# Kernel optimization log

Measured on AMD Instinct MI355X. Metric: run time of the kernel, lower is better.

Reference implementation:

```python
import jax, jax.numpy as jnp
import numpy as np

N_NODES = 50000
N_EDGES = 800000
IN_DIM = 128
HID = 64
HEADS = 4
OUT_DIM = 20
NUM_GRAPHS = 64
NEG_SLOPE = 0.2  # PyG GATConv default leaky_relu slope


def _xavier(key, shape):
    fan_in, fan_out = shape[-1], shape[0]
    lim = float(np.sqrt(6.0 / (fan_in + fan_out)))
    return jax.random.uniform(key, shape, jnp.float32, -lim, lim)


def setup_inputs() -> dict:
    key = jax.random.key(0)
    ks = jax.random.split(key, 12)
    x = jax.random.normal(ks[0], (N_NODES, IN_DIM), jnp.float32)
    edge_index = jax.random.randint(ks[1], (2, N_EDGES), 0, N_NODES, jnp.int32)
    batch = jnp.sort(jax.random.randint(ks[2], (N_NODES,), 0, NUM_GRAPHS, jnp.int32))
    return {
        "x": x,
        "edge_index": edge_index,
        "batch": batch,
        # conv1: in -> HEADS*HID, concat
        "W1": _xavier(ks[3], (HEADS * HID, IN_DIM)),
        "a_src1": _xavier(ks[4], (HEADS, HID)),
        "a_dst1": _xavier(ks[5], (HEADS, HID)),
        "b1": jnp.zeros((HEADS * HID,), jnp.float32),
        # conv2: HEADS*HID -> HID, 1 head
        "W2": _xavier(ks[6], (HID, HEADS * HID)),
        "a_src2": _xavier(ks[7], (1, HID)),
        "a_dst2": _xavier(ks[8], (1, HID)),
        "b2": jnp.zeros((HID,), jnp.float32),
        "fc_W": _xavier(ks[9], (OUT_DIM, HID)),
        "fc_b": jnp.zeros((OUT_DIM,), jnp.float32),
    }


def _gat_conv(x, src, dst, W, a_src, a_dst, b, heads):
    """PyG GATConv: linear -> per-edge LeakyReLU attention -> softmax over
    incoming edges of each target node -> weighted scatter-sum. Self-loops
    are already included in (src, dst). Dropout omitted (eval mode)."""
    n = x.shape[0]
    h = (x @ W.T).reshape(n, heads, -1)            # [N, H, C]
    alpha_s = jnp.einsum("nhc,hc->nh", h, a_src)   # [N, H]
    alpha_d = jnp.einsum("nhc,hc->nh", h, a_dst)
    e = jax.nn.leaky_relu(alpha_s[src] + alpha_d[dst], NEG_SLOPE)  # [E, H]
    # numerically stable segment softmax over dst
    e_max = jax.ops.segment_max(e, dst, num_segments=n)
    e = jnp.exp(e - e_max[dst])
    denom = jax.ops.segment_sum(e, dst, num_segments=n)
    alpha = e / (denom[dst] + 1e-16)               # [E, H]
    msg = h[src] * alpha[..., None]                # [E, H, C]
    out = jax.ops.segment_sum(msg, dst, num_segments=n)  # [N, H, C]
    return out.reshape(n, -1) + b                  # concat heads


def reference(x, edge_index, batch, W1, a_src1, a_dst1, b1,
              W2, a_src2, a_dst2, b2, fc_W, fc_b):
    n = x.shape[0]
    loops = jnp.arange(n, dtype=edge_index.dtype)
    src = jnp.concatenate([edge_index[0], loops])  # add self-loops (PyG default)
    dst = jnp.concatenate([edge_index[1], loops])
    h = jax.nn.elu(_gat_conv(x, src, dst, W1, a_src1, a_dst1, b1, HEADS))
    h = jax.nn.elu(_gat_conv(h, src, dst, W2, a_src2, a_dst2, b2, 1))
    pooled = jax.ops.segment_max(h, batch, num_segments=NUM_GRAPHS)  # [G, HID]
    return pooled @ fc_W.T + fc_b                  # [G, OUT_DIM]
```

## Files before the change

### kernel.cpp

```cpp
#include <hip/hip_runtime.h>
#include <hip/hip_bf16.h>

#define N_NODES_C 50000
#define N_EDGES_C 800000
#define IN_DIM_C  128
#define HID_C     64
#define HEADS_C   4
#define OUT_DIM_C 20
#define NUM_GRAPHS_C 64
#define NEG_SLOPE 0.2f
#define SCAN_BLOCKS 196

typedef __attribute__((ext_vector_type(8))) short bf16x8;
typedef __attribute__((ext_vector_type(4))) float f32x4;
typedef __attribute__((ext_vector_type(2))) float f32x2;

__device__ __forceinline__ float lrelu(float t){ return t > 0.f ? t : NEG_SLOPE*t; }
__device__ __forceinline__ float elu1(float t){ return t > 0.f ? t : __expf(t)-1.f; }
__device__ __forceinline__ ushort f2bf(float f){
  unsigned u = __float_as_uint(f);
  return (ushort)((u + 0x7fffu + ((u>>16)&1u)) >> 16);
}
__device__ __forceinline__ float bflo(unsigned u){ return __uint_as_float(u<<16); }
__device__ __forceinline__ float bfhi(unsigned u){ return __uint_as_float(u & 0xffff0000u); }
__device__ __forceinline__ float bfs(ushort u){ return __uint_as_float(((unsigned)u)<<16); }

__global__ void hist_kernel(const int* __restrict__ ei, int* __restrict__ cursor){
  int e = blockIdx.x*256 + threadIdx.x;
  if (e < N_EDGES_C) atomicAdd(&cursor[ei[N_EDGES_C + e]], 1);
}

__global__ __launch_bounds__(256) void reduce_counts(const int* __restrict__ cursor, int* __restrict__ blockSums){
  int i = blockIdx.x*256 + threadIdx.x;
  int c = (i < N_NODES_C) ? cursor[i] : 0;
  #pragma unroll
  for(int d=32; d>=1; d>>=1) c += __shfl_xor(c, d);
  __shared__ int s4[4];
  int lane = threadIdx.x & 63, wv = threadIdx.x >> 6;
  if(lane==0) s4[wv] = c;
  __syncthreads();
  if(threadIdx.x==0) blockSums[blockIdx.x] = s4[0]+s4[1]+s4[2]+s4[3];
}

__global__ __launch_bounds__(256) void scan_sums(int* __restrict__ blockSums){
  __shared__ int sh[256];
  int t = threadIdx.x;
  int v = (t < SCAN_BLOCKS) ? blockSums[t] : 0;
  sh[t] = v; __syncthreads();
  #pragma unroll
  for(int off=1; off<256; off<<=1){
    int u = (t>=off) ? sh[t-off] : 0;
    __syncthreads();
    sh[t] += u;
    __syncthreads();
  }
  if(t < SCAN_BLOCKS) blockSums[t] = sh[t] - v;
}

__global__ __launch_bounds__(256) void scan_block(int* __restrict__ cursor, const int* __restrict__ blockSums,
                                                  int* __restrict__ offsets){
  __shared__ int sh[256];
  int t = threadIdx.x;
  int i = blockIdx.x*256 + t;
  int c = (i < N_NODES_C) ? cursor[i] : 0;
  sh[t] = c; __syncthreads();
  #pragma unroll
  for(int off=1; off<256; off<<=1){
    int u = (t>=off) ? sh[t-off] : 0;
    __syncthreads();
    sh[t] += u;
    __syncthreads();
  }
  int excl = sh[t] - c;
  int pref = blockSums[blockIdx.x] + excl;
  if(i < N_NODES_C){
    offsets[i] = pref;
    cursor[i]  = pref;
    if(i == N_NODES_C-1) offsets[N_NODES_C] = pref + c;
  }
}

__global__ void fill_kernel(const int* __restrict__ ei, int* __restrict__ cursor,
                            int* __restrict__ adj){
  int e = blockIdx.x*256 + threadIdx.x;
  if (e >= N_EDGES_C) return;
  int sI = ei[e]; int d = ei[N_EDGES_C + e];
  int p = atomicAdd(&cursor[d], 1);
  adj[p] = sI;
}

__global__ __launch_bounds__(256) void wperm_kernel(const float* __restrict__ W1, const float* __restrict__ W2,
    ushort* __restrict__ Wp1h, ushort* __restrict__ Wp1l,
    ushort* __restrict__ Wp2h, ushort* __restrict__ Wp2l){
  int i = blockIdx.x*256 + threadIdx.x;
  const float* src; ushort *dh, *dl; int gidx;
  if(i < 4096){
    int kc = i>>10, oc = (i>>6)&15, l = i&63;
    src = W1 + (size_t)(oc*16 + (l&15))*IN_DIM_C + kc*32 + (l>>4)*8;
    dh = Wp1h; dl = Wp1l; gidx = i;
  } else if(i < 4096+2048){
    int i2 = i - 4096;
    int kc = i2>>8, oc = (i2>>6)&3, l = i2&63;
    src = W2 + (size_t)(oc*16 + (l&15))*256 + kc*32 + (l>>4)*8;
    dh = Wp2h; dl = Wp2l; gidx = i2;
  } else return;
  ushort h8[8], l8[8];
  #pragma unroll
  for(int j=0;j<8;j++){
    float f = src[j];
    ushort h = f2bf(f);
    h8[j] = h; l8[j] = f2bf(f - bfs(h));
  }
  #pragma unroll
  for(int j=0;j<8;j++){ dh[gidx*8+j] = h8[j]; dl[gidx*8+j] = l8[j]; }
}

#define HS1_STRIDE 260
__global__ __launch_bounds__(256) void lin1_mfma(const float* __restrict__ x,
    const ushort* __restrict__ Wp1h, const ushort* __restrict__ Wp1l,
    const float* __restrict__ aS, const float* __restrict__ aD,
    ushort* __restrict__ h1, float* __restrict__ as1, float* __restrict__ ad1){
  __shared__ ushort hs[64*HS1_STRIDE];
  int t = threadIdx.x, w = t>>6, l = t&63;
  int n0b = blockIdx.x*64;
  int n0 = n0b + w*16;
  bool active = (n0 < N_NODES_C);
  int row = l & 15, kg = l >> 4;
  if(active){
    bf16x8 ah[4], al[4];
    int gn = n0 + row; if(gn > N_NODES_C-1) gn = N_NODES_C-1;
    const float* xrow = x + (size_t)gn*IN_DIM_C + kg*8;
    #pragma unroll
    for(int kc=0;kc<4;kc++){
      float4 f0 = *(const float4*)(xrow + kc*32);
      float4 f1 = *(const float4*)(xrow + kc*32 + 4);
      float fv[8] = {f0.x,f0.y,f0.z,f0.w,f1.x,f1.y,f1.z,f1.w};
      #pragma unroll
      for(int j=0;j<8;j++){
        ushort h = f2bf(fv[j]);
        float r = fv[j] - bfs(h);
        ah[kc][j] = (short)h;
        al[kc][j] = (short)f2bf(r);
      }
    }
    const bf16x8* Wh = (const bf16x8*)Wp1h + l;
    const bf16x8* Wl = (const bf16x8*)Wp1l + l;
    f32x4 acc[16];
    #pragma unroll
    for(int oc=0;oc<16;oc++){
      f32x4 a = {0.f,0.f,0.f,0.f};
      const bf16x8* ph = Wh + oc*64;
      const bf16x8* pl = Wl + oc*64;
      #pragma unroll
      for(int kc=0;kc<4;kc++){
        bf16x8 bh = ph[kc*1024];
        bf16x8 bl = pl[kc*1024];
        a = __builtin_amdgcn_mfma_f32_16x16x32_bf16(ah[kc], bh, a, 0, 0, 0);
        a = __builtin_amdgcn_mfma_f32_16x16x32_bf16(ah[kc], bl, a, 0, 0, 0);
        a = __builtin_amdgcn_mfma_f32_16x16x32_bf16(al[kc], bh, a, 0, 0, 0);
      }
      acc[oc] = a;
    }
    #pragma unroll
    for(int h=0;h<4;h++){
      float ps0=0.f,ps1=0.f,ps2=0.f,ps3=0.f, pd0=0.f,pd1=0.f,pd2=0.f,pd3=0.f;
      #pragma unroll
      for(int oi=0;oi<4;oi++){
        int oc = h*4 + oi;
        float as_ = aS[oc*16 + row];
        float ad_ = aD[oc*16 + row];
        ps0 = fmaf(acc[oc][0], as_, ps0); pd0 = fmaf(acc[oc][0], ad_, pd0);
        ps1 = fmaf(acc[oc][1], as_, ps1); pd1 = fmaf(acc[oc][1], ad_, pd1);
        ps2 = fmaf(acc[oc][2], as_, ps2); pd2 = fmaf(acc[oc][2], ad_, pd2);
        ps3 = fmaf(acc[oc][3], as_, ps3); pd3 = fmaf(acc[oc][3], ad_, pd3);
      }
      #pragma unroll
      for(int d=1; d<16; d<<=1){
        ps0 += __shfl_xor(ps0,d); ps1 += __shfl_xor(ps1,d);
        ps2 += __shfl_xor(ps2,d); ps3 += __shfl_xor(ps3,d);
        pd0 += __shfl_xor(pd0,d); pd1 += __shfl_xor(pd1,d);
        pd2 += __shfl_xor(pd2,d); pd3 += __shfl_xor(pd3,d);
      }
      if(row==0){
        int nb4 = (n0 + kg*4)*4 + h;
        as1[nb4+0] = ps0; as1[nb4+4] = ps1; as1[nb4+8] = ps2; as1[nb4+12] = ps3;
        ad1[nb4+0] = pd0; ad1[nb4+4] = pd1; ad1[nb4+8] = pd2; ad1[nb4+12] = pd3;
      }
    }
    #pragma unroll
    for(int oc=0;oc<16;oc++){
      #pragma unroll
      for(int r=0;r<4;r++){
        hs[(w*16 + kg*4 + r)*HS1_STRIDE + oc*16 + row] = f2bf(acc[oc][r]);
      }
    }
  }
  __syncthreads();
  int nvalid = N_NODES_C - n0b; if(nvalid > 64) nvalid = 64;
  for(int i=t; i<nvalid*32; i+=256){
    int r = i>>5, c = i&31;
    ((uint4*)(h1 + (size_t)(n0b+r)*256))[c] = *(const uint4*)(hs + r*HS1_STRIDE + c*8);
  }
}

__global__ __launch_bounds__(256) void agg1_kernel(const int* __restrict__ offsets, const int* __restrict__ adj,
    const ushort* __restrict__ h1,
    const float* __restrict__ as1, const float* __restrict__ ad1,
    const float* __restrict__ b1, float* __restrict__ out1){
  int wv = threadIdx.x>>6, lane = threadIdx.x&63;
  int v = blockIdx.x*4 + wv;
  int head = lane>>4;
  int start = offsets[v], end = offsets[v+1];
  float adh = ad1[(v<<2)+head];
  float ash = as1[(v<<2)+head];
  float wself = __expf(lrelu(ash+adh));
  float denom = wself;
  const char* hb = (const char*)h1;
  unsigned loff = ((unsigned)lane)<<3;
  uint2 pv = *(const uint2*)(hb + ((((unsigned)v)<<9) + loff));
  f32x2 acc01 = {wself*bflo(pv.x), wself*bfhi(pv.x)};
  f32x2 acc23 = {wself*bflo(pv.y), wself*bfhi(pv.y)};
  int i = start;
  for(; i+8 <= end; i += 8){
    int s0 = adj[i],   s1 = adj[i+1], s2 = adj[i+2], s3 = adj[i+3];
    int s4 = adj[i+4], s5 = adj[i+5], s6 = adj[i+6], s7 = adj[i+7];
    float a0 = as1[(s0<<2)+head], a1 = as1[(s1<<2)+head];
    float a2 = as1[(s2<<2)+head], a3 = as1[(s3<<2)+head];
    float a4 = as1[(s4<<2)+head], a5 = as1[(s5<<2)+head];
    float a6 = as1[(s6<<2)+head], a7 = as1[(s7<<2)+head];
    uint2 p0 = *(const uint2*)(hb + ((((unsigned)s0)<<9) + loff));
    uint2 p1 = *(const uint2*)(hb + ((((unsigned)s1)<<9) + loff));
    uint2 p2 = *(const uint2*)(hb + ((((unsigned)s2)<<9) + loff));
    uint2 p3 = *(const uint2*)(hb + ((((unsigned)s3)<<9) + loff));
    uint2 p4 = *(const uint2*)(hb + ((((unsigned)s4)<<9) + loff));
    uint2 p5 = *(const uint2*)(hb + ((((unsigned)s5)<<9) + loff));
    uint2 p6 = *(const uint2*)(hb + ((((unsigned)s6)<<9) + loff));
    uint2 p7 = *(const uint2*)(hb + ((((unsigned)s7)<<9) + loff));
    float w0 = __expf(lrelu(a0+adh)), w1 = __expf(lrelu(a1+adh));
    float w2 = __expf(lrelu(a2+adh)), w3 = __expf(lrelu(a3+adh));
    float w4 = __expf(lrelu(a4+adh)), w5 = __expf(lrelu(a5+adh));
    float w6 = __expf(lrelu(a6+adh)), w7 = __expf(lrelu(a7+adh));
    denom += ((w0+w1)+(w2+w3)) + ((w4+w5)+(w6+w7));
    f32x2 W;
    W.x = w0; W.y = w0;
    acc01 = __builtin_elementwise_fma(W, (f32x2){bflo(p0.x), bfhi(p0.x)}, acc01);
    acc23 = __builtin_elementwise_fma(W, (f32x2){bflo(p0.y), bfhi(p0.y)}, acc23);
    W.x = w1; W.y = w1;
    acc01 = __builtin_elementwise_fma(W, (f32x2){bflo(p1.x), bfhi(p1.x)}, acc01);
    acc23 = __builtin_elementwise_fma(W, (f32x2){bflo(p1.y), bfhi(p1.y)}, acc23);
    W.x = w2; W.y = w2;
    acc01 = __builtin_elementwise_fma(W, (f32x2){bflo(p2.x), bfhi(p2.x)}, acc01);
    acc23 = __builtin_elementwise_fma(W, (f32x2){bflo(p2.y), bfhi(p2.y)}, acc23);
    W.x = w3; W.y = w3;
    acc01 = __builtin_elementwise_fma(W, (f32x2){bflo(p3.x), bfhi(p3.x)}, acc01);
    acc23 = __builtin_elementwise_fma(W, (f32x2){bflo(p3.y), bfhi(p3.y)}, acc23);
    W.x = w4; W.y = w4;
    acc01 = __builtin_elementwise_fma(W, (f32x2){bflo(p4.x), bfhi(p4.x)}, acc01);
    acc23 = __builtin_elementwise_fma(W, (f32x2){bflo(p4.y), bfhi(p4.y)}, acc23);
    W.x = w5; W.y = w5;
    acc01 = __builtin_elementwise_fma(W, (f32x2){bflo(p5.x), bfhi(p5.x)}, acc01);
    acc23 = __builtin_elementwise_fma(W, (f32x2){bflo(p5.y), bfhi(p5.y)}, acc23);
    W.x = w6; W.y = w6;
    acc01 = __builtin_elementwise_fma(W, (f32x2){bflo(p6.x), bfhi(p6.x)}, acc01);
    acc23 = __builtin_elementwise_fma(W, (f32x2){bflo(p6.y), bfhi(p6.y)}, acc23);
    W.x = w7; W.y = w7;
    acc01 = __builtin_elementwise_fma(W, (f32x2){bflo(p7.x), bfhi(p7.x)}, acc01);
    acc23 = __builtin_elementwise_fma(W, (f32x2){bflo(p7.y), bfhi(p7.y)}, acc23);
  }
  for(; i < end; i++){
    int s0 = adj[i];
    float a0 = as1[(s0<<2)+head];
    uint2 p0 = *(const uint2*)(hb + ((((unsigned)s0)<<9) + loff));
    float w0 = __expf(lrelu(a0+adh));
    denom += w0;
    f32x2 W; W.x = w0; W.y = w0;
    acc01 = __builtin_elementwise_fma(W, (f32x2){bflo(p0.x), bfhi(p0.x)}, acc01);
    acc23 = __builtin_elementwise_fma(W, (f32x2){bflo(p0.y), bfhi(p0.y)}, acc23);
  }
  float inv = 1.f/(denom + 1e-16f);
  float4 bv = *(const float4*)(b1 + (lane<<2));
  float4 r;
  r.x = elu1(acc01.x*inv + bv.x);
  r.y = elu1(acc01.y*inv + bv.y);
  r.z = elu1(acc23.x*inv + bv.z);
  r.w = elu1(acc23.y*inv + bv.w);
  *(float4*)(out1 + ((size_t)v<<8) + (lane<<2)) = r;
}

#define HS2_STRIDE 68
__global__ __launch_bounds__(256) void lin2_mfma(const float* __restrict__ in,
    const ushort* __restrict__ Wp2h, const ushort* __restrict__ Wp2l,
    const float* __restrict__ aS, const float* __restrict__ aD,
    ushort* __restrict__ h2, float* __restrict__ as2, float* __restrict__ ad2){
  __shared__ ushort hs[64*HS2_STRIDE];
  int t = threadIdx.x, w = t>>6, l = t&63;
  int n0b = blockIdx.x*64;
  int n0 = n0b + w*16;
  bool active = (n0 < N_NODES_C);
  int row = l & 15, kg = l >> 4;
  if(active){
    bf16x8 ah[8], al[8];
    int gn = n0 + row; if(gn > N_NODES_C-1) gn = N_NODES_C-1;
    const float* xrow = in + (size_t)gn*256 + kg*8;
    #pragma unroll
    for(int kc=0;kc<8;kc++){
      float4 f0 = *(const float4*)(xrow + kc*32);
      float4 f1 = *(const float4*)(xrow + kc*32 + 4);
      float fv[8] = {f0.x,f0.y,f0.z,f0.w,f1.x,f1.y,f1.z,f1.w};
      #pragma unroll
      for(int j=0;j<8;j++){
        ushort h = f2bf(fv[j]);
        float r = fv[j] - bfs(h);
        ah[kc][j] = (short)h;
        al[kc][j] = (short)f2bf(r);
      }
    }
    const bf16x8* Wh = (const bf16x8*)Wp2h + l;
    const bf16x8* Wl = (const bf16x8*)Wp2l + l;
    f32x4 acc[4];
    #pragma unroll
    for(int oc=0;oc<4;oc++){
      f32x4 a = {0.f,0.f,0.f,0.f};
      const bf16x8* ph = Wh + oc*64;
      const bf16x8* pl = Wl + oc*64;
      #pragma unroll
      for(int kc=0;kc<8;kc++){
        bf16x8 bh = ph[kc*256];
        bf16x8 bl = pl[kc*256];
        a = __builtin_amdgcn_mfma_f32_16x16x32_bf16(ah[kc], bh, a, 0, 0, 0);
        a = __builtin_amdgcn_mfma_f32_16x16x32_bf16(ah[kc], bl, a, 0, 0, 0);
        a = __builtin_amdgcn_mfma_f32_16x16x32_bf16(al[kc], bh, a, 0, 0, 0);
      }
      acc[oc] = a;
    }
    {
      float ps0=0.f,ps1=0.f,ps2=0.f,ps3=0.f, pd0=0.f,pd1=0.f,pd2=0.f,pd3=0.f;
      #pragma unroll
      for(int oc=0;oc<4;oc++){
        float as_ = aS[oc*16 + row];
        float ad_ = aD[oc*16 + row];
        ps0 = fmaf(acc[oc][0], as_, ps0); pd0 = fmaf(acc[oc][0], ad_, pd0);
        ps1 = fmaf(acc[oc][1], as_, ps1); pd1 = fmaf(acc[oc][1], ad_, pd1);
        ps2 = fmaf(acc[oc][2], as_, ps2); pd2 = fmaf(acc[oc][2], ad_, pd2);
        ps3 = fmaf(acc[oc][3], as_, ps3); pd3 = fmaf(acc[oc][3], ad_, pd3);
      }
      #pragma unroll
      for(int d=1; d<16; d<<=1){
        ps0 += __shfl_xor(ps0,d); ps1 += __shfl_xor(ps1,d);
        ps2 += __shfl_xor(ps2,d); ps3 += __shfl_xor(ps3,d);
        pd0 += __shfl_xor(pd0,d); pd1 += __shfl_xor(pd1,d);
        pd2 += __shfl_xor(pd2,d); pd3 += __shfl_xor(pd3,d);
      }
      if(row==0){
        int n = n0 + kg*4;
        as2[n+0] = ps0; as2[n+1] = ps1; as2[n+2] = ps2; as2[n+3] = ps3;
        ad2[n+0] = pd0; ad2[n+1] = pd1; ad2[n+2] = pd2; ad2[n+3] = pd3;
      }
    }
    #pragma unroll
    for(int oc=0;oc<4;oc++){
      #pragma unroll
      for(int r=0;r<4;r++){
        hs[(w*16 + kg*4 + r)*HS2_STRIDE + oc*16 + row] = f2bf(acc[oc][r]);
      }
    }
  }
  __syncthreads();
  int nvalid = N_NODES_C - n0b; if(nvalid > 64) nvalid = 64;
  for(int i=t; i<nvalid*8; i+=256){
    int r = i>>3, c = i&7;
    ((uint4*)(h2 + (size_t)(n0b+r)*64))[c] = *(const uint4*)(hs + r*HS2_STRIDE + c*8);
  }
}

__global__ __launch_bounds__(256) void agg2_kernel(const int* __restrict__ offsets, const int* __restrict__ adj,
    const ushort* __restrict__ h2,
    const float* __restrict__ as2, const float* __restrict__ ad2,
    const float* __restrict__ b2, float* __restrict__ out2){
  int wv = threadIdx.x>>6, lane = threadIdx.x&63;
  int v = blockIdx.x*4 + wv;
  int half = lane>>5, sl = lane&31;
  int start = offsets[v], end = offsets[v+1];
  float adv = ad2[v], asv = as2[v];
  float wself = __expf(lrelu(asv+adv));
  const unsigned* hu = (const unsigned*)h2;
  float denom = half ? 0.f : wself;
  f32x2 acc = {0.f, 0.f};
  if(!half){
    unsigned us = hu[(((unsigned)v)<<5) + sl];
    acc.x = wself*bflo(us); acc.y = wself*bfhi(us);
  }
  int i = start + half;
  for(; i+2 < end; i += 4){
    int sA = adj[i], sB = adj[i+2];
    float aA = as2[sA], aB = as2[sB];
    unsigned uA = hu[(((unsigned)sA)<<5) + sl];
    unsigned uB = hu[(((unsigned)sB)<<5) + sl];
    float wA = __expf(lrelu(aA+adv));
    float wB = __expf(lrelu(aB+adv));
    denom += wA + wB;
    f32x2 W;
    W.x = wA; W.y = wA;
    acc = __builtin_elementwise_fma(W, (f32x2){bflo(uA), bfhi(uA)}, acc);
    W.x = wB; W.y = wB;
    acc = __builtin_elementwise_fma(W, (f32x2){bflo(uB), bfhi(uB)}, acc);
  }
  for(; i < end; i += 2){
    int s = adj[i];
    float wg = __expf(lrelu(as2[s]+adv));
    unsigned u = hu[(((unsigned)s)<<5) + sl];
    denom += wg;
    f32x2 W; W.x = wg; W.y = wg;
    acc = __builtin_elementwise_fma(W, (f32x2){bflo(u), bfhi(u)}, acc);
  }
  acc.x += __shfl_xor(acc.x, 32);
  acc.y += __shfl_xor(acc.y, 32);
  denom += __shfl_xor(denom, 32);
  if(!half){
    float inv = 1.f/(denom + 1e-16f);
    float2 bv = *(const float2*)(b2 + sl*2);
    float2 r;
    r.x = elu1(acc.x*inv + bv.x);
    r.y = elu1(acc.y*inv + bv.y);
    *(float2*)(out2 + (((size_t)v)<<6) + sl*2) = r;
  }
}

__global__ __launch_bounds__(256) void pool_fc_kernel(const float* __restrict__ out2, const int* __restrict__ batch,
    const float* __restrict__ fcW, const float* __restrict__ fcb, float* __restrict__ out){
  int g = blockIdx.x;
  int tid=threadIdx.x; int c = tid&63; int slot = tid>>6;
  int lo=0, hi=N_NODES_C;
  while(lo<hi){ int mid=(lo+hi)>>1; if(batch[mid] < g) lo=mid+1; else hi=mid; }
  int start=lo;
  hi=N_NODES_C;
  while(lo<hi){ int mid=(lo+hi)>>1; if(batch[mid] < g+1) lo=mid+1; else hi=mid; }
  int end=lo;
  float mm = -INFINITY;
  #pragma unroll 4
  for(int n=start+slot; n<end; n+=4) mm = fmaxf(mm, out2[(size_t)n*64+c]);
  __shared__ float sred[4][64];
  sred[slot][c]=mm;
  __syncthreads();
  if(tid < 64){
    float p = fmaxf(fmaxf(sred[0][tid],sred[1][tid]), fmaxf(sred[2][tid],sred[3][tid]));
    sred[0][tid]=p;
  }
  __syncthreads();
  if(tid < OUT_DIM_C){
    float acc = fcb[tid];
    #pragma unroll
    for(int cc=0;cc<64;cc++) acc = fmaf(sred[0][cc], fcW[tid*64+cc], acc);
    out[g*OUT_DIM_C + tid] = acc;
  }
}

extern "C" void kernel_launch(void* const* d_in, const int* in_sizes, int n_in,
                              void* d_out, int out_size, void* d_ws, size_t ws_size,
                              hipStream_t stream) {
  const float* x   = (const float*)d_in[0];
  const int*   ei  = (const int*)  d_in[1];
  const int*   bat = (const int*)  d_in[2];
  const float* W1  = (const float*)d_in[3];
  const float* aS1 = (const float*)d_in[4];
  const float* aD1 = (const float*)d_in[5];
  const float* b1  = (const float*)d_in[6];
  const float* W2  = (const float*)d_in[7];
  const float* aS2 = (const float*)d_in[8];
  const float* aD2 = (const float*)d_in[9];
  const float* b2  = (const float*)d_in[10];
  const float* fcW = (const float*)d_in[11];
  const float* fcb = (const float*)d_in[12];
  float* out = (float*)d_out;

  char* w = (char*)d_ws;
  size_t off = 0;
  auto alloc = [&](size_t bytes)->char* {
    char* p = w + off; off = (off + bytes + 255) & ~(size_t)255; return p;
  };
  int* offsets   = (int*)alloc((N_NODES_C+1)*sizeof(int));
  int* cursor    = (int*)alloc((size_t)N_NODES_C*sizeof(int));
  int* blockSums = (int*)alloc(SCAN_BLOCKS*sizeof(int));
  int* adj       = (int*)alloc((size_t)(N_EDGES_C+8)*sizeof(int));
  ushort* Wp1h   = (ushort*)alloc((size_t)4096*8*sizeof(ushort));
  ushort* Wp1l   = (ushort*)alloc((size_t)4096*8*sizeof(ushort));
  ushort* Wp2h   = (ushort*)alloc((size_t)2048*8*sizeof(ushort));
  ushort* Wp2l   = (ushort*)alloc((size_t)2048*8*sizeof(ushort));
  ushort* h1     = (ushort*)alloc((size_t)N_NODES_C*256*sizeof(ushort));
  float* as1     = (float*)alloc((size_t)N_NODES_C*4*sizeof(float));
  float* ad1     = (float*)alloc((size_t)N_NODES_C*4*sizeof(float));
  float* out1    = (float*)alloc((size_t)N_NODES_C*256*sizeof(float));
  ushort* h2  = h1;
  float* as2  = as1;
  float* ad2  = ad1;
  float* out2 = out1;
  (void)ws_size; (void)in_sizes; (void)n_in; (void)out_size;

  hipMemsetAsync(cursor, 0, (size_t)N_NODES_C*sizeof(int), stream);
  hist_kernel<<<(N_EDGES_C+255)/256, 256, 0, stream>>>(ei, cursor);
  reduce_counts<<<SCAN_BLOCKS, 256, 0, stream>>>(cursor, blockSums);
  scan_sums<<<1, 256, 0, stream>>>(blockSums);
  scan_block<<<SCAN_BLOCKS, 256, 0, stream>>>(cursor, blockSums, offsets);
  fill_kernel<<<(N_EDGES_C+255)/256, 256, 0, stream>>>(ei, cursor, adj);
  wperm_kernel<<<24, 256, 0, stream>>>(W1, W2, Wp1h, Wp1l, Wp2h, Wp2l);

  lin1_mfma<<<(N_NODES_C+63)/64, 256, 0, stream>>>(x, Wp1h, Wp1l, aS1, aD1, h1, as1, ad1);
  agg1_kernel<<<N_NODES_C/4, 256, 0, stream>>>(offsets, adj, h1, as1, ad1, b1, out1);
  lin2_mfma<<<(N_NODES_C+63)/64, 256, 0, stream>>>(out1, Wp2h, Wp2l, aS2, aD2, h2, as2, ad2);
  agg2_kernel<<<N_NODES_C/4, 256, 0, stream>>>(offsets, adj, h2, as2, ad2, b2, out2);
  pool_fc_kernel<<<NUM_GRAPHS_C, 256, 0, stream>>>(out2, bat, fcW, fcb, out);
}
```

Before: 395.1 us.

## Split GAT aggregation across channel slices and edge-parallel lane groups

Both aggregation kernels now launch more blocks, with each block handling a 32-channel slice of the feature row. Within a wave, four 16-lane groups walk interleaved edges, and their partial sums are combined with cross-lane shuffles. This aims to raise parallelism and memory-level concurrency for the gather-bound aggregation. The cost is that adjacency lists and attention scalars are re-read once per slice, and each gather is narrower. LeakyReLU is also rewritten as a branchless fmax.

Result: slower. 521.3 us (+31.9%).

```diff
diff --git a/kernel.cpp b/kernel.cpp
--- a/kernel.cpp
+++ b/kernel.cpp
@@ -15,7 +15,7 @@
 typedef __attribute__((ext_vector_type(4))) float f32x4;
 typedef __attribute__((ext_vector_type(2))) float f32x2;
 
-__device__ __forceinline__ float lrelu(float t){ return t > 0.f ? t : NEG_SLOPE*t; }
+__device__ __forceinline__ float lrelu(float t){ return fmaxf(t, NEG_SLOPE*t); }
 __device__ __forceinline__ float elu1(float t){ return t > 0.f ? t : __expf(t)-1.f; }
 __device__ __forceinline__ ushort f2bf(float f){
   unsigned u = __float_as_uint(f);
@@ -207,84 +207,60 @@
     const ushort* __restrict__ h1,
     const float* __restrict__ as1, const float* __restrict__ ad1,
     const float* __restrict__ b1, float* __restrict__ out1){
+  int b = blockIdx.x;
+  int slice = b & 7;
+  int vgrp = b >> 3;
   int wv = threadIdx.x>>6, lane = threadIdx.x&63;
-  int v = blockIdx.x*4 + wv;
-  int head = lane>>4;
+  int grp = lane>>4, cl = lane&15;
+  int v = vgrp*4 + wv;
+  int head = slice >> 1;
   int start = offsets[v], end = offsets[v+1];
   float adh = ad1[(v<<2)+head];
   float ash = as1[(v<<2)+head];
+  const unsigned* hrow = (const unsigned*)h1;
+  unsigned choff = slice*16 + cl;
   float wself = __expf(lrelu(ash+adh));
-  float denom = wself;
-  const char* hb = (const char*)h1;
-  unsigned loff = ((unsigned)lane)<<3;
-  uint2 pv = *(const uint2*)(hb + ((((unsigned)v)<<9) + loff));
-  f32x2 acc01 = {wself*bflo(pv.x), wself*bfhi(pv.x)};
-  f32x2 acc23 = {wself*bflo(pv.y), wself*bfhi(pv.y)};
-  int i = start;
-  for(; i+8 <= end; i += 8){
-    int s0 = adj[i],   s1 = adj[i+1], s2 = adj[i+2], s3 = adj[i+3];
-    int s4 = adj[i+4], s5 = adj[i+5], s6 = adj[i+6], s7 = adj[i+7];
-    float a0 = as1[(s0<<2)+head], a1 = as1[(s1<<2)+head];
-    float a2 = as1[(s2<<2)+head], a3 = as1[(s3<<2)+head];
-    float a4 = as1[(s4<<2)+head], a5 = as1[(s5<<2)+head];
-    float a6 = as1[(s6<<2)+head], a7 = as1[(s7<<2)+head];
-    uint2 p0 = *(const uint2*)(hb + ((((unsigned)s0)<<9) + loff));
-    uint2 p1 = *(const uint2*)(hb + ((((unsigned)s1)<<9) + loff));
-    uint2 p2 = *(const uint2*)(hb + ((((unsigned)s2)<<9) + loff));
-    uint2 p3 = *(const uint2*)(hb + ((((unsigned)s3)<<9) + loff));
-    uint2 p4 = *(const uint2*)(hb + ((((unsigned)s4)<<9) + loff));
-    uint2 p5 = *(const uint2*)(hb + ((((unsigned)s5)<<9) + loff));
-    uint2 p6 = *(const uint2*)(hb + ((((unsigned)s6)<<9) + loff));
-    uint2 p7 = *(const uint2*)(hb + ((((unsigned)s7)<<9) + loff));
-    float w0 = __expf(lrelu(a0+adh)), w1 = __expf(lrelu(a1+adh));
-    float w2 = __expf(lrelu(a2+adh)), w3 = __expf(lrelu(a3+adh));
-    float w4 = __expf(lrelu(a4+adh)), w5 = __expf(lrelu(a5+adh));
-    float w6 = __expf(lrelu(a6+adh)), w7 = __expf(lrelu(a7+adh));
-    denom += ((w0+w1)+(w2+w3)) + ((w4+w5)+(w6+w7));
+  float denom = (grp==0) ? wself : 0.f;
+  f32x2 acc = {0.f,0.f};
+  if(grp==0){
+    unsigned u = hrow[((unsigned)v<<7) + choff];
+    acc.x = wself*bflo(u); acc.y = wself*bfhi(u);
+  }
+  int i = start + grp;
+  for(; i+4 < end; i += 8){
+    int sA = adj[i], sB = adj[i+4];
+    float aA = as1[(sA<<2)+head], aB = as1[(sB<<2)+head];
+    unsigned uA = hrow[((unsigned)sA<<7) + choff];
+    unsigned uB = hrow[((unsigned)sB<<7) + choff];
+    float wA = __expf(lrelu(aA+adh));
+    float wB = __expf(lrelu(aB+adh));
+    denom += wA + wB;
     f32x2 W;
-    W.x = w0; W.y = w0;
-    acc01 = __builtin_elementwise_fma(W, (f32x2){bflo(p0.x), bfhi(p0.x)}, acc01);
-    acc23 = __builtin_elementwise_fma(W, (f32x2){bflo(p0.y), bfhi(p0.y)}, acc23);
-    W.x = w1; W.y = w1;
-    acc01 = __builtin_elementwise_fma(W, (f32x2){bflo(p1.x), bfhi(p1.x)}, acc01);
-    acc23 = __builtin_elementwise_fma(W, (f32x2){bflo(p1.y), bfhi(p1.y)}, acc23);
-    W.x = w2; W.y = w2;
-    acc01 = __builtin_elementwise_fma(W, (f32x2){bflo(p2.x), bfhi(p2.x)}, acc01);
-    acc23 = __builtin_elementwise_fma(W, (f32x2){bflo(p2.y), bfhi(p2.y)}, acc23);
-    W.x = w3; W.y = w3;
-    acc01 = __builtin_elementwise_fma(W, (f32x2){bflo(p3.x), bfhi(p3.x)}, acc01);
-    acc23 = __builtin_elementwise_fma(W, (f32x2){bflo(p3.y), bfhi(p3.y)}, acc23);
-    W.x = w4; W.y = w4;
-    acc01 = __builtin_elementwise_fma(W, (f32x2){bflo(p4.x), bfhi(p4.x)}, acc01);
-    acc23 = __builtin_elementwise_fma(W, (f32x2){bflo(p4.y), bfhi(p4.y)}, acc23);
-    W.x = w5; W.y = w5;
-    acc01 = __builtin_elementwise_fma(W, (f32x2){bflo(p5.x), bfhi(p5.x)}, acc01);
-    acc23 = __builtin_elementwise_fma(W, (f32x2){bflo(p5.y), bfhi(p5.y)}, acc23);
-    W.x = w6; W.y = w6;
-    acc01 = __builtin_elementwise_fma(W, (f32x2){bflo(p6.x), bfhi(p6.x)}, acc01);
-    acc23 = __builtin_elementwise_fma(W, (f32x2){bflo(p6.y), bfhi(p6.y)}, acc23);
-    W.x = w7; W.y = w7;
-    acc01 = __builtin_elementwise_fma(W, (f32x2){bflo(p7.x), bfhi(p7.x)}, acc01);
-    acc23 = __builtin_elementwise_fma(W, (f32x2){bflo(p7.y), bfhi(p7.y)}, acc23);
-  }
-  for(; i < end; i++){
-    int s0 = adj[i];
-    float a0 = as1[(s0<<2)+head];
-    uint2 p0 = *(const uint2*)(hb + ((((unsigned)s0)<<9) + loff));
-    float w0 = __expf(lrelu(a0+adh));
-    denom += w0;
-    f32x2 W; W.x = w0; W.y = w0;
-    acc01 = __builtin_elementwise_fma(W, (f32x2){bflo(p0.x), bfhi(p0.x)}, acc01);
-    acc23 = __builtin_elementwise_fma(W, (f32x2){bflo(p0.y), bfhi(p0.y)}, acc23);
-  }
-  float inv = 1.f/(denom + 1e-16f);
-  float4 bv = *(const float4*)(b1 + (lane<<2));
-  float4 r;
-  r.x = elu1(acc01.x*inv + bv.x);
-  r.y = elu1(acc01.y*inv + bv.y);
-  r.z = elu1(acc23.x*inv + bv.z);
-  r.w = elu1(acc23.y*inv + bv.w);
-  *(float4*)(out1 + ((size_t)v<<8) + (lane<<2)) = r;
+    W.x=wA; W.y=wA;
+    acc = __builtin_elementwise_fma(W, (f32x2){bflo(uA),bfhi(uA)}, acc);
+    W.x=wB; W.y=wB;
+    acc = __builtin_elementwise_fma(W, (f32x2){bflo(uB),bfhi(uB)}, acc);
+  }
+  for(; i < end; i += 4){
+    int s = adj[i];
+    float a = as1[(s<<2)+head];
+    unsigned u = hrow[((unsigned)s<<7) + choff];
+    float wgt = __expf(lrelu(a+adh));
+    denom += wgt;
+    f32x2 W; W.x=wgt; W.y=wgt;
+    acc = __builtin_elementwise_fma(W, (f32x2){bflo(u),bfhi(u)}, acc);
+  }
+  acc.x += __shfl_xor(acc.x, 16); acc.y += __shfl_xor(acc.y, 16); denom += __shfl_xor(denom, 16);
+  acc.x += __shfl_xor(acc.x, 32); acc.y += __shfl_xor(acc.y, 32); denom += __shfl_xor(denom, 32);
+  if(grp==0){
+    float inv = 1.f/(denom + 1e-16f);
+    int ch = slice*32 + cl*2;
+    float2 bv = *(const float2*)(b1 + ch);
+    float2 r;
+    r.x = elu1(acc.x*inv + bv.x);
+    r.y = elu1(acc.y*inv + bv.y);
+    *(float2*)(out1 + ((size_t)v<<8) + ch) = r;
+  }
 }
 
 #define HS2_STRIDE 68
@@ -377,52 +353,57 @@
     const ushort* __restrict__ h2,
     const float* __restrict__ as2, const float* __restrict__ ad2,
     const float* __restrict__ b2, float* __restrict__ out2){
+  int b = blockIdx.x;
+  int slice = b & 1;
+  int vgrp = b >> 1;
   int wv = threadIdx.x>>6, lane = threadIdx.x&63;
-  int v = blockIdx.x*4 + wv;
-  int half = lane>>5, sl = lane&31;
+  int grp = lane>>4, cl = lane&15;
+  int v = vgrp*4 + wv;
   int start = offsets[v], end = offsets[v+1];
   float adv = ad2[v], asv = as2[v];
+  const unsigned* hrow = (const unsigned*)h2;
+  unsigned choff = slice*16 + cl;
   float wself = __expf(lrelu(asv+adv));
-  const unsigned* hu = (const unsigned*)h2;
-  float denom = half ? 0.f : wself;
-  f32x2 acc = {0.f, 0.f};
-  if(!half){
-    unsigned us = hu[(((unsigned)v)<<5) + sl];
-    acc.x = wself*bflo(us); acc.y = wself*bfhi(us);
-  }
-  int i = start + half;
-  for(; i+2 < end; i += 4){
-    int sA = adj[i], sB = adj[i+2];
+  float denom = (grp==0) ? wself : 0.f;
+  f32x2 acc = {0.f,0.f};
+  if(grp==0){
+    unsigned u = hrow[((unsigned)v<<5) + choff];
+    acc.x = wself*bflo(u); acc.y = wself*bfhi(u);
+  }
+  int i = start + grp;
+  for(; i+4 < end; i += 8){
+    int sA = adj[i], sB = adj[i+4];
     float aA = as2[sA], aB = as2[sB];
-    unsigned uA = hu[(((unsigned)sA)<<5) + sl];
-    unsigned uB = hu[(((unsigned)sB)<<5) + sl];
+    unsigned uA = hrow[((unsigned)sA<<5) + choff];
+    unsigned uB = hrow[((unsigned)sB<<5) + choff];
     float wA = __expf(lrelu(aA+adv));
     float wB = __expf(lrelu(aB+adv));
     denom += wA + wB;
     f32x2 W;
-    W.x = wA; W.y = wA;
-    acc = __builtin_elementwise_fma(W, (f32x2){bflo(uA), bfhi(uA)}, acc);
-    W.x = wB; W.y = wB;
-    acc = __builtin_elementwise_fma(W, (f32x2){bflo(uB), bfhi(uB)}, acc);
-  }
-  for(; i < end; i += 2){
+    W.x=wA; W.y=wA;
+    acc = __builtin_elementwise_fma(W, (f32x2){bflo(uA),bfhi(uA)}, acc);
+    W.x=wB; W.y=wB;
+    acc = __builtin_elementwise_fma(W, (f32x2){bflo(uB),bfhi(uB)}, acc);
+  }
+  for(; i < end; i += 4){
     int s = adj[i];
-    float wg = __expf(lrelu(as2[s]+adv));
-    unsigned u = hu[(((unsigned)s)<<5) + sl];
-    denom += wg;
-    f32x2 W; W.x = wg; W.y = wg;
-    acc = __builtin_elementwise_fma(W, (f32x2){bflo(u), bfhi(u)}, acc);
-  }
-  acc.x += __shfl_xor(acc.x, 32);
-  acc.y += __shfl_xor(acc.y, 32);
-  denom += __shfl_xor(denom, 32);
-  if(!half){
+    float a = as2[s];
+    unsigned u = hrow[((unsigned)s<<5) + choff];
+    float wgt = __expf(lrelu(a+adv));
+    denom += wgt;
+    f32x2 W; W.x=wgt; W.y=wgt;
+    acc = __builtin_elementwise_fma(W, (f32x2){bflo(u),bfhi(u)}, acc);
+  }
+  acc.x += __shfl_xor(acc.x, 16); acc.y += __shfl_xor(acc.y, 16); denom += __shfl_xor(denom, 16);
+  acc.x += __shfl_xor(acc.x, 32); acc.y += __shfl_xor(acc.y, 32); denom += __shfl_xor(denom, 32);
+  if(grp==0){
     float inv = 1.f/(denom + 1e-16f);
-    float2 bv = *(const float2*)(b2 + sl*2);
+    int ch = slice*32 + cl*2;
+    float2 bv = *(const float2*)(b2 + ch);
     float2 r;
     r.x = elu1(acc.x*inv + bv.x);
     r.y = elu1(acc.y*inv + bv.y);
-    *(float2*)(out2 + (((size_t)v)<<6) + sl*2) = r;
+    *(float2*)(out2 + ((size_t)v<<6) + ch) = r;
   }
 }
 
@@ -505,8 +486,8 @@
   wperm_kernel<<<24, 256, 0, stream>>>(W1, W2, Wp1h, Wp1l, Wp2h, Wp2l);
 
   lin1_mfma<<<(N_NODES_C+63)/64, 256, 0, stream>>>(x, Wp1h, Wp1l, aS1, aD1, h1, as1, ad1);
-  agg1_kernel<<<N_NODES_C/4, 256, 0, stream>>>(offsets, adj, h1, as1, ad1, b1, out1);
+  agg1_kernel<<<(N_NODES_C/4)*8, 256, 0, stream>>>(offsets, adj, h1, as1, ad1, b1, out1);
   lin2_mfma<<<(N_NODES_C+63)/64, 256, 0, stream>>>(out1, Wp2h, Wp2l, aS2, aD2, h2, as2, ad2);
-  agg2_kernel<<<N_NODES_C/4, 256, 0, stream>>>(offsets, adj, h2, as2, ad2, b2, out2);
+  agg2_kernel<<<(N_NODES_C/4)*2, 256, 0, stream>>>(offsets, adj, h2, as2, ad2, b2, out2);
   pool_fc_kernel<<<NUM_GRAPHS_C, 256, 0, stream>>>(out2, bat, fcW, fcb, out);
 }
```
